# Optimization experiments

Measured on AMD Instinct MI355X. Metric: run time of the kernel, lower is better.

## Reference

```python
import jax, jax.numpy as jnp
import numpy as np

B, N, DIM = 2, 2048, 2048
H, DH = 16, 128            # heads, dim_head; dim_inner = H*DH = 2048
SOFTCAP = 50.0
SCALE = DH ** -0.5


def setup_inputs() -> dict:
    key = jax.random.key(0)
    k1, k2, k3, k4 = jax.random.split(key, 4)
    s = 1.0 / np.sqrt(DIM)
    x = jax.random.normal(k1, (B, N, DIM), dtype=jnp.float32)
    w_qkv = jax.random.normal(k2, (DIM, 3 * H * DH), dtype=jnp.float32) * s
    w_gates = jax.random.normal(k3, (DIM, H), dtype=jnp.float32) * s
    w_out = jax.random.normal(k4, (H * DH, DIM), dtype=jnp.float32) * s
    return {"x": x, "w_qkv": w_qkv, "w_gates": w_gates, "w_out": w_out}


def reference(x, w_qkv, w_gates, w_out):
    b, n, _ = x.shape
    # to_qkv: Linear then 'b n (qkv h d) -> qkv b h n d'
    qkv = (x @ w_qkv).reshape(b, n, 3, H, DH).transpose(2, 0, 3, 1, 4)
    q, k, v = qkv[0], qkv[1], qkv[2]            # each [b, h, n, d]
    q = q * SCALE
    sim = jnp.einsum('bhid,bhjd->bhij', q, k)   # [b, h, n, n]
    sim = jnp.tanh(sim / SOFTCAP) * SOFTCAP     # softclamp
    mask_value = -jnp.finfo(sim.dtype).max
    causal_mask = jnp.triu(jnp.ones((n, n), dtype=bool), 1)
    sim = jnp.where(causal_mask, mask_value, sim)
    attn = jax.nn.softmax(sim, axis=-1)         # dropout = 0.0 (eval)
    out = jnp.einsum('bhij,bhjd->bhid', attn, v)
    # gating: 'b n h -> b h n 1' then sigmoid
    gates = jax.nn.sigmoid(x @ w_gates)         # [b, n, h]
    out = out * gates.transpose(0, 2, 1)[..., None]
    # to_out: 'b h n d -> b n (h d)' then Linear
    out = out.transpose(0, 2, 1, 3).reshape(b, n, H * DH) @ w_out
    return out
```

## Files before the change

### kernel.cpp

```cpp
#include <hip/hip_runtime.h>
#include <hip/hip_bf16.h>
#include <math.h>


typedef __attribute__((ext_vector_type(8))) __bf16 bf16x8;
typedef __attribute__((ext_vector_type(4))) __bf16 bf16x4;
typedef __attribute__((ext_vector_type(4))) float f32x4;

#define MFMA_BF16(a, b, c) __builtin_amdgcn_mfma_f32_16x16x32_bf16((a), (b), (c), 0, 0, 0)

#define NB 2
#define NSEQ 2048
#define NDIM 2048
#define NH 16
#define NDH 128
#define SCALE_Q 0.08838834764831845f

#define AS1 __attribute__((address_space(1)))
#define AS3 __attribute__((address_space(3)))
static __device__ __forceinline__ void gload_lds16(const void* g, void* l) {
  __builtin_amdgcn_global_load_lds((AS1 const void*)g, (AS3 void*)l, 16, 0, 0);
}

static __device__ __forceinline__ unsigned pack2_bf16(float a, float b) {
  unsigned short ua = __builtin_bit_cast(unsigned short, (__bf16)a);
  unsigned short ub = __builtin_bit_cast(unsigned short, (__bf16)b);
  return (unsigned)ua | ((unsigned)ub << 16);
}

__global__ __launch_bounds__(256) void cvt_bf16_kernel(const float* __restrict__ in,
                                                       __bf16* __restrict__ out) {
  int i = blockIdx.x * 256 + threadIdx.x;
  float4 v = reinterpret_cast<const float4*>(in)[i];
  bf16x4 o;
  o[0] = (__bf16)v.x; o[1] = (__bf16)v.y; o[2] = (__bf16)v.z; o[3] = (__bf16)v.w;
  reinterpret_cast<bf16x4*>(out)[i] = o;
}

__global__ __launch_bounds__(256) void transpose_cvt_kernel(const float* __restrict__ in,
                                                            __bf16* __restrict__ out,
                                                            int K, int C) {
  __shared__ float tile[32][33];
  int c0 = blockIdx.x * 32, k0 = blockIdx.y * 32;
  int t = threadIdx.x;
  int lc = t & 31, lr = t >> 5;
#pragma unroll
  for (int rr = 0; rr < 4; ++rr)
    tile[lr + rr * 8][lc] = in[(size_t)(k0 + lr + rr * 8) * C + c0 + lc];
  __syncthreads();
#pragma unroll
  for (int rr = 0; rr < 4; ++rr)
    out[(size_t)(c0 + lr + rr * 8) * K + k0 + lc] = (__bf16)tile[lc][lr + rr * 8];
}

template <int BN> struct SmemG {
  __bf16 A[2][2][128][32];
  __bf16 B[2][2][BN][32];
};

template <int BN>
static __device__ __forceinline__ void stage_half(const __bf16* __restrict__ Ab,
                                                  const __bf16* __restrict__ Bb,
                                                  SmemG<BN>* S, int buf, int ks,
                                                  int kt, int w, int lane) {
  constexpr int LB = BN / 128;
  {
    int gid = w * 64 + lane;
    int row = gid >> 2, gc = gid & 3;
    int sg = gc ^ ((row >> 1) & 3);
    gload_lds16(Ab + (size_t)row * 2048 + kt * 64 + ks * 32 + sg * 8,
                &S->A[buf][ks][0][0] + (size_t)(w * 64) * 8);
  }
#pragma unroll
  for (int j = 0; j < LB; ++j) {
    int gid = j * 512 + w * 64 + lane;
    int row = gid >> 2, gc = gid & 3;
    int sg = gc ^ ((row >> 1) & 3);
    gload_lds16(Bb + (size_t)row * 2048 + kt * 64 + ks * 32 + sg * 8,
                &S->B[buf][ks][0][0] + (size_t)(j * 512 + w * 64) * 8);
  }
}

static __device__ __forceinline__ const bf16x8* fragp(const __bf16* base, int row, int g) {
  return (const bf16x8*)(base + row * 32 + (g ^ ((row >> 1) & 3)) * 8);
}

template <int BN>
static __device__ __forceinline__ void gemm128_core(const __bf16* __restrict__ Abase,
                                                    const __bf16* __restrict__ Bbase,
                                                    SmemG<BN>* S,
                                                    f32x4 (*acc)[BN / 64]) {
  constexpr int NF = BN / 64;
  constexpr int LB = BN / 128;
  int tid = threadIdx.x;
  int w = tid >> 6, lane = tid & 63;
  int ln15 = lane & 15, g = lane >> 4;
  int wr = w >> 2, wc = w & 3;

#pragma unroll
  for (int i = 0; i < 4; ++i)
#pragma unroll
    for (int j = 0; j < NF; ++j) acc[i][j] = (f32x4){0.f, 0.f, 0.f, 0.f};

  stage_half<BN>(Abase, Bbase, S, 0, 0, 0, w, lane);
  stage_half<BN>(Abase, Bbase, S, 0, 1, 0, w, lane);

  for (int t = 0; t < 32; ++t) {
    int bf = t & 1, tb = bf ^ 1;
    int ts = (t < 31) ? t + 1 : 31;
#pragma unroll
    for (int ks = 0; ks < 2; ++ks) {
      stage_half<BN>(Abase, Bbase, S, tb, ks, ts, w, lane);
      if constexpr (LB == 3)
        asm volatile("s_waitcnt vmcnt(8)" ::: "memory");
      else
        asm volatile("s_waitcnt vmcnt(6)" ::: "memory");
      __builtin_amdgcn_s_barrier();
      const __bf16* SA = &S->A[bf][ks][0][0];
      const __bf16* SB = &S->B[bf][ks][0][0];
      bf16x8 af[4], bfr[NF];
#pragma unroll
      for (int nf = 0; nf < NF; ++nf) {
        int row = wc * (BN / 4) + nf * 16 + ln15;
        bfr[nf] = *fragp(SB, row, g);
      }
#pragma unroll
      for (int mf = 0; mf < 4; ++mf) {
        int row = wr * 64 + mf * 16 + ln15;
        af[mf] = *fragp(SA, row, g);
      }
      __builtin_amdgcn_s_setprio(1);
#pragma unroll
      for (int mf = 0; mf < 4; ++mf)
#pragma unroll
        for (int nf = 0; nf < NF; ++nf)
          acc[mf][nf] = MFMA_BF16(af[mf], bfr[nf], acc[mf][nf]);
      __builtin_amdgcn_s_setprio(0);
    }
  }
  asm volatile("s_waitcnt vmcnt(0)" ::: "memory");
}

__global__ __launch_bounds__(512) void gemm_qkv128(const __bf16* __restrict__ A,
                                                   const __bf16* __restrict__ Bt,
                                                   __bf16* __restrict__ qb,
                                                   __bf16* __restrict__ kb,
                                                   __bf16* __restrict__ vtb) {
  __shared__ __align__(1024) SmemG<384> S;
  int sblk = blockIdx.x;
  int x = sblk & 7, i = sblk >> 3;
  int m0 = (i >> 1) * 128;
  int n0 = (2 * x + (i & 1)) * 384;
  f32x4 acc[4][6];
  gemm128_core<384>(A + (size_t)m0 * 2048, Bt + (size_t)n0 * 2048, &S, acc);

  int tid = threadIdx.x;
  int w = tid >> 6, lane = tid & 63;
  int ln15 = lane & 15, g = lane >> 4;
  int wr = w >> 2, wc = w & 3;
#pragma unroll
  for (int nf = 0; nf < 6; ++nf) {
    int ng = n0 + wc * 96 + nf * 16 + ln15;
    int qkv = ng >> 11;
    int h = (ng >> 7) & 15;
    int d = ng & 127;
#pragma unroll
    for (int mf = 0; mf < 4; ++mf)
#pragma unroll
      for (int rr = 0; rr < 4; ++rr) {
        int m = m0 + wr * 64 + mf * 16 + g * 4 + rr;
        int b = m >> 11, n = m & 2047;
        int bh = b * NH + h;
        float v = acc[mf][nf][rr];
        if (qkv == 0)
          qb[((size_t)bh * NSEQ + n) * NDH + d] = (__bf16)(v * SCALE_Q);
        else if (qkv == 1)
          kb[((size_t)bh * NSEQ + n) * NDH + d] = (__bf16)v;
        else
          vtb[((size_t)bh * NDH + d) * NSEQ + n] = (__bf16)v;
      }
  }
}

__global__ __launch_bounds__(512) void gemm_out128(const __bf16* __restrict__ A,
                                                   const __bf16* __restrict__ Bt,
                                                   float* __restrict__ out) {
  __shared__ __align__(1024) SmemG<256> S;
  int sblk = blockIdx.x;
  int x = sblk & 7, i = sblk >> 3;
  int m0 = i * 128;
  int n0 = x * 256;
  f32x4 acc[4][4];
  gemm128_core<256>(A + (size_t)m0 * 2048, Bt + (size_t)n0 * 2048, &S, acc);

  int tid = threadIdx.x;
  int w = tid >> 6, lane = tid & 63;
  int ln15 = lane & 15, g = lane >> 4;
  int wr = w >> 2, wc = w & 3;
#pragma unroll
  for (int mf = 0; mf < 4; ++mf)
#pragma unroll
    for (int nf = 0; nf < 4; ++nf)
#pragma unroll
      for (int rr = 0; rr < 4; ++rr) {
        int m = m0 + wr * 64 + mf * 16 + g * 4 + rr;
        int c = n0 + wc * 64 + nf * 16 + ln15;
        out[(size_t)m * NDIM + c] = acc[mf][nf][rr];
      }
}

__global__ __launch_bounds__(256) void gates_kernel(const float* __restrict__ x,
                                                    const float* __restrict__ wg,
                                                    float* __restrict__ gates) {
  __shared__ float red[64];
  int row = blockIdx.x;
  int tid = threadIdx.x;
  float acc[16];
#pragma unroll
  for (int h = 0; h < 16; ++h) acc[h] = 0.f;
  const float* xr = x + (size_t)row * NDIM;
  for (int k = tid; k < NDIM; k += 256) {
    float xv = xr[k];
    const float* wr = wg + (size_t)k * NH;
#pragma unroll
    for (int h = 0; h < 16; ++h) acc[h] += xv * wr[h];
  }
  int w = tid >> 6, lane = tid & 63;
#pragma unroll
  for (int h = 0; h < 16; ++h) {
    float v = acc[h];
#pragma unroll
    for (int off = 32; off; off >>= 1) v += __shfl_down(v, off);
    if (lane == 0) red[w * 16 + h] = v;
  }
  __syncthreads();
  if (tid < 16) {
    float s = red[tid] + red[16 + tid] + red[32 + tid] + red[48 + tid];
    int b = row >> 11, n = row & 2047;
    gates[((size_t)(b * NH + tid)) * NSEQ + n] = 1.f / (1.f + expf(-s));
  }
}

static __device__ __forceinline__ void softcap_p(const f32x4* accS, float (*p)[4],
                                                 float& l_r, int j0, int q0s,
                                                 bool diag, int ln15, int g) {
#pragma unroll
  for (int jt = 0; jt < 4; ++jt)
#pragma unroll
    for (int r = 0; r < 4; ++r) {
      float e2 = __expf(accS[jt][r] * 0.04f);
      float cap = 50.f - __fdividef(100.f, e2 + 1.f);
      float pv = __expf(cap - 12.f);
      if (diag && (j0 + jt * 16 + g * 4 + r > q0s + ln15)) pv = 0.f;
      p[jt][r] = pv;
      l_r += pv;
    }
}

static __device__ __forceinline__ bf16x8 build_pa(const float (*p)[4], int c,
                                                  int lane_lo, int lane_hi, int g) {
  unsigned P0w0 = pack2_bf16(p[2 * c][0], p[2 * c][1]);
  unsigned P0w1 = pack2_bf16(p[2 * c][2], p[2 * c][3]);
  unsigned P1w0 = pack2_bf16(p[2 * c + 1][0], p[2 * c + 1][1]);
  unsigned P1w1 = pack2_bf16(p[2 * c + 1][2], p[2 * c + 1][3]);
  unsigned a0 = (unsigned)__shfl((int)P0w0, lane_lo);
  unsigned a1 = (unsigned)__shfl((int)P0w1, lane_lo);
  unsigned b0 = (unsigned)__shfl((int)P1w0, lane_lo);
  unsigned b1 = (unsigned)__shfl((int)P1w1, lane_lo);
  unsigned c0 = (unsigned)__shfl((int)P0w0, lane_hi);
  unsigned c1 = (unsigned)__shfl((int)P0w1, lane_hi);
  unsigned e0 = (unsigned)__shfl((int)P1w0, lane_hi);
  unsigned e1 = (unsigned)__shfl((int)P1w1, lane_hi);
  union { unsigned u[4]; bf16x8 v; } pu;
  pu.u[0] = (g < 2) ? a0 : b0;
  pu.u[1] = (g < 2) ? a1 : b1;
  pu.u[2] = (g < 2) ? c0 : e0;
  pu.u[3] = (g < 2) ? c1 : e1;
  return pu.v;
}

static __device__ __forceinline__ void attn_tile2(const __bf16* __restrict__ Kl,
                                                  const __bf16* __restrict__ Vl,
                                                  const bf16x8* qfh, const bf16x8* qfl,
                                                  f32x4* acc_h, f32x4* acc_l,
                                                  float& l_h, float& l_l,
                                                  int j0, int q0h, int q0l,
                                                  bool diag_h, bool diag_l, bool do_lo,
                                                  int ln15, int g) {
  f32x4 sh[4], sl[4];
#pragma unroll
  for (int jt = 0; jt < 4; ++jt) {
    sh[jt] = (f32x4){0.f, 0.f, 0.f, 0.f};
    sl[jt] = (f32x4){0.f, 0.f, 0.f, 0.f};
  }
  __builtin_amdgcn_s_setprio(1);
#pragma unroll
  for (int jt = 0; jt < 4; ++jt)
#pragma unroll
    for (int kc = 0; kc < 4; ++kc) {
      int row = jt * 16 + ln15;
      int bc = (kc * 64 + g * 16) ^ ((row & 7) << 4);
      bf16x8 kf = *reinterpret_cast<const bf16x8*>(Kl + row * 128 + (bc >> 1));
      sh[jt] = MFMA_BF16(kf, qfh[kc], sh[jt]);
      if (do_lo) sl[jt] = MFMA_BF16(kf, qfl[kc], sl[jt]);
    }
  __builtin_amdgcn_s_setprio(0);
  float ph[4][4], pl[4][4];
  softcap_p(sh, ph, l_h, j0, q0h, diag_h, ln15, g);
  if (do_lo) softcap_p(sl, pl, l_l, j0, q0l, diag_l, ln15, g);
  int lane_lo = ln15 + 32 * (g & 1);
  int lane_hi = lane_lo + 16;
#pragma unroll
  for (int c = 0; c < 2; ++c) {
    bf16x8 pah = build_pa(ph, c, lane_lo, lane_hi, g);
    bf16x8 pal = build_pa(pl, c, lane_lo, lane_hi, g);
    __builtin_amdgcn_s_setprio(1);
#pragma unroll
    for (int d0 = 0; d0 < 8; ++d0) {
      int d = d0 * 16 + ln15;
      int bc = (c * 64 + g * 16) ^ ((d & 7) << 4);
      bf16x8 vf = *reinterpret_cast<const bf16x8*>(Vl + d * 64 + (bc >> 1));
      acc_h[d0] = MFMA_BF16(pah, vf, acc_h[d0]);
      if (do_lo) acc_l[d0] = MFMA_BF16(pal, vf, acc_l[d0]);
    }
    __builtin_amdgcn_s_setprio(0);
  }
}

__global__ __launch_bounds__(256, 2) void attn_kernel(const __bf16* __restrict__ qb,
                                                      const __bf16* __restrict__ kb,
                                                      const __bf16* __restrict__ vtb,
                                                      const float* __restrict__ gates,
                                                      __bf16* __restrict__ og) {
  __shared__ __align__(1024) __bf16 Kl[2][64 * 128];
  __shared__ __align__(1024) __bf16 Vl[2][128 * 64];
  int tid = threadIdx.x;
  int w = tid >> 6, lane = tid & 63;
  int ln15 = lane & 15, g = lane >> 4;
  int bx = blockIdx.x;
  int lo = bx & 15, bh = bx >> 4;
  int hi = 31 - lo;
  const __bf16* qh = qb + (size_t)bh * NSEQ * NDH;
  const __bf16* kh = kb + (size_t)bh * NSEQ * NDH;
  const __bf16* vh = vtb + (size_t)bh * NDH * NSEQ;

  int q0h = hi * 64 + w * 16;
  int q0l = lo * 64 + w * 16;
  bf16x8 qfh[4], qfl[4];
#pragma unroll
  for (int kc = 0; kc < 4; ++kc) {
    qfh[kc] = *reinterpret_cast<const bf16x8*>(qh + (size_t)(q0h + ln15) * NDH + kc * 32 + g * 8);
    qfl[kc] = *reinterpret_cast<const bf16x8*>(qh + (size_t)(q0l + ln15) * NDH + kc * 32 + g * 8);
  }

  f32x4 acc_h[8], acc_l[8];
#pragma unroll
  for (int d0 = 0; d0 < 8; ++d0) {
    acc_h[d0] = (f32x4){0.f, 0.f, 0.f, 0.f};
    acc_l[d0] = (f32x4){0.f, 0.f, 0.f, 0.f};
  }
  float l_h = 0.f, l_l = 0.f;

  auto stage = [&](int t, int buf) {
    int j0 = t * 64;
#pragma unroll
    for (int i = 0; i < 4; ++i) {
      int gi = (i * 4 + w) * 64 + lane;
      int kr = gi >> 4, kcs = gi & 15;
      int kc_ = kcs ^ (kr & 7);
      gload_lds16(kh + (size_t)(j0 + kr) * NDH + kc_ * 8, &Kl[buf][(i * 4 + w) * 512]);
      int vr = gi >> 3, vcs = gi & 7;
      int vc_ = vcs ^ (vr & 7);
      gload_lds16(vh + (size_t)vr * NSEQ + j0 + vc_ * 8, &Vl[buf][(i * 4 + w) * 512]);
    }
  };

  stage(0, 0);
  for (int t = 0; t <= hi; ++t) {
    int cb = t & 1;
    if (t < hi) {
      stage(t + 1, cb ^ 1);
      asm volatile("s_waitcnt vmcnt(8)" ::: "memory");
    } else {
      asm volatile("s_waitcnt vmcnt(0)" ::: "memory");
    }
    __builtin_amdgcn_s_barrier();
    attn_tile2(&Kl[cb][0], &Vl[cb][0], qfh, qfl, acc_h, acc_l, l_h, l_l,
               t * 64, q0h, q0l, t == hi, t == lo, t <= lo, ln15, g);
    __builtin_amdgcn_s_barrier();
  }

  l_h += __shfl_xor(l_h, 16); l_h += __shfl_xor(l_h, 32);
  l_l += __shfl_xor(l_l, 16); l_l += __shfl_xor(l_l, 32);

  int b = bh >> 4, h = bh & 15;
#pragma unroll
  for (int set = 0; set < 2; ++set) {
    int q0s = set ? q0l : q0h;
    f32x4* acc = set ? acc_l : acc_h;
    float lr = set ? l_l : l_h;
    float gv[4];
#pragma unroll
    for (int r = 0; r < 4; ++r) {
      float lv = __shfl(lr, g * 4 + r);
      int row = q0s + g * 4 + r;
      gv[r] = gates[(size_t)bh * NSEQ + row] / lv;
    }
#pragma unroll
    for (int d0 = 0; d0 < 8; ++d0)
#pragma unroll
      for (int r = 0; r < 4; ++r) {
        int row = q0s + g * 4 + r;
        og[((size_t)(b * NSEQ + row)) * NDIM + h * NDH + d0 * 16 + ln15] =
            (__bf16)(acc[d0][r] * gv[r]);
      }
  }
}

extern "C" void kernel_launch(void* const* d_in, const int* in_sizes, int n_in,
                              void* d_out, int out_size, void* d_ws, size_t ws_size,
                              hipStream_t stream) {
  const float* x = (const float*)d_in[0];
  const float* w_qkv = (const float*)d_in[1];
  const float* w_gates = (const float*)d_in[2];
  const float* w_out = (const float*)d_in[3];
  float* out = (float*)d_out;
  char* ws = (char*)d_ws;

  __bf16* x_bf   = (__bf16*)(ws + 0);
  __bf16* wqkv_t = (__bf16*)(ws + 16777216);
  __bf16* wout_t = (__bf16*)(ws + 41943040);
  __bf16* q_buf  = (__bf16*)(ws + 50331648);
  __bf16* k_buf  = (__bf16*)(ws + 67108864);
  __bf16* vt_buf = (__bf16*)(ws + 83886080);
  float*  gates  = (float*)(ws + 100663296);
  __bf16* attn_g = (__bf16*)(ws + 100925440);

  cvt_bf16_kernel<<<8192, 256, 0, stream>>>(x, x_bf);
  transpose_cvt_kernel<<<dim3(192, 64), 256, 0, stream>>>(w_qkv, wqkv_t, 2048, 6144);
  transpose_cvt_kernel<<<dim3(64, 64), 256, 0, stream>>>(w_out, wout_t, 2048, 2048);
  gemm_qkv128<<<512, 512, 0, stream>>>(x_bf, wqkv_t, q_buf, k_buf, vt_buf);
  gates_kernel<<<4096, 256, 0, stream>>>(x, w_gates, gates);
  attn_kernel<<<512, 256, 0, stream>>>(q_buf, k_buf, vt_buf, gates, attn_g);
  gemm_out128<<<256, 512, 0, stream>>>(attn_g, wout_t, out);
}
```

Before: 353.7 us.

## Replace QKV GEMM with 256x384 tile and triple-buffered K-32 LDS pipeline

Replaces the 128x384-tile QKV projection GEMM with a new kernel that computes 256x384 tiles (8x6 MFMA fragments per wave) over 256 blocks. It uses a 3-stage ring of 32-wide K slices in LDS, staged with direct global-to-LDS loads two iterations ahead and one barrier per step. The larger M tile halves B-operand reloads per output and the deeper pipeline aims to hide load latency. In exchange it uses more accumulator registers per thread and launches half as many blocks, which may cut occupancy or leave CUs underused.

```diff
diff --git a/kernel.cpp b/kernel.cpp
--- a/kernel.cpp
+++ b/kernel.cpp
@@ -51,6 +51,111 @@
 #pragma unroll
   for (int rr = 0; rr < 4; ++rr)
     out[(size_t)(c0 + lr + rr * 8) * K + k0 + lc] = (__bf16)tile[lc][lr + rr * 8];
+}
+
+struct SmemQ {
+  __bf16 T[3][640][32];
+};
+
+static __device__ __forceinline__ const bf16x8* fragq(const __bf16* base, int row, int g) {
+  return (const bf16x8*)(base + row * 32 + (g ^ ((row >> 1) & 3)) * 8);
+}
+
+__global__ __launch_bounds__(512, 2) void gemm_qkv256b(const __bf16* __restrict__ A,
+                                                       const __bf16* __restrict__ Bt,
+                                                       __bf16* __restrict__ qb,
+                                                       __bf16* __restrict__ kb,
+                                                       __bf16* __restrict__ vtb) {
+  __shared__ __align__(1024) SmemQ S;
+  int sblk = blockIdx.x;
+  int x = sblk & 7, i = sblk >> 3;
+  int m0 = (i >> 1) * 256;
+  int n0 = (2 * x + (i & 1)) * 384;
+  const __bf16* Ab = A + (size_t)m0 * 2048;
+  const __bf16* Bb = Bt + (size_t)n0 * 2048;
+
+  int tid = threadIdx.x;
+  int w = tid >> 6, lane = tid & 63;
+  int ln15 = lane & 15, g = lane >> 4;
+  int wr = w >> 2, wc = w & 3;
+  int lr4 = lane >> 2, l3 = lane & 3;
+
+  auto stage = [&](int kt, int rb) {
+#pragma unroll
+    for (int j = 0; j < 5; ++j) {
+      int k = w + 8 * j;
+      int row = k * 16 + lr4;
+      int sg = l3 ^ ((row >> 1) & 3);
+      const __bf16* src = (k < 16)
+          ? Ab + (size_t)row * 2048 + kt * 32 + sg * 8
+          : Bb + (size_t)(row - 256) * 2048 + kt * 32 + sg * 8;
+      gload_lds16(src, &S.T[rb][k * 16][0]);
+    }
+  };
+
+  f32x4 acc[8][6];
+#pragma unroll
+  for (int a = 0; a < 8; ++a)
+#pragma unroll
+    for (int nf = 0; nf < 6; ++nf) acc[a][nf] = (f32x4){0.f, 0.f, 0.f, 0.f};
+
+  stage(0, 0);
+  stage(1, 1);
+  for (int t = 0; t < 64; ++t) {
+    int rb = t % 3;
+    asm volatile("s_waitcnt vmcnt(5)" ::: "memory");
+    __builtin_amdgcn_s_barrier();
+    asm volatile("" ::: "memory");
+    int ts = (t < 62) ? t + 2 : 63;
+    stage(ts, (t + 2) % 3);
+    const __bf16* Sb = &S.T[rb][0][0];
+    bf16x8 bfr[6];
+#pragma unroll
+    for (int nf = 0; nf < 6; ++nf) {
+      int row = 256 + wc * 96 + nf * 16 + ln15;
+      bfr[nf] = *fragq(Sb, row, g);
+    }
+#pragma unroll
+    for (int mh = 0; mh < 2; ++mh) {
+      bf16x8 af[4];
+#pragma unroll
+      for (int a = 0; a < 4; ++a) {
+        int row = wr * 128 + (mh * 4 + a) * 16 + ln15;
+        af[a] = *fragq(Sb, row, g);
+      }
+      __builtin_amdgcn_s_setprio(1);
+#pragma unroll
+      for (int a = 0; a < 4; ++a)
+#pragma unroll
+        for (int nf = 0; nf < 6; ++nf)
+          acc[mh * 4 + a][nf] = MFMA_BF16(af[a], bfr[nf], acc[mh * 4 + a][nf]);
+      __builtin_amdgcn_s_setprio(0);
+    }
+  }
+  asm volatile("s_waitcnt vmcnt(0)" ::: "memory");
+
+#pragma unroll
+  for (int nf = 0; nf < 6; ++nf) {
+    int ng = n0 + wc * 96 + nf * 16 + ln15;
+    int qkv = ng >> 11;
+    int h = (ng >> 7) & 15;
+    int d = ng & 127;
+#pragma unroll
+    for (int mf = 0; mf < 8; ++mf)
+#pragma unroll
+      for (int rr = 0; rr < 4; ++rr) {
+        int m = m0 + wr * 128 + mf * 16 + g * 4 + rr;
+        int b = m >> 11, n = m & 2047;
+        int bh = b * NH + h;
+        float v = acc[mf][nf][rr];
+        if (qkv == 0)
+          qb[((size_t)bh * NSEQ + n) * NDH + d] = (__bf16)(v * SCALE_Q);
+        else if (qkv == 1)
+          kb[((size_t)bh * NSEQ + n) * NDH + d] = (__bf16)v;
+        else
+          vtb[((size_t)bh * NDH + d) * NSEQ + n] = (__bf16)v;
+      }
+  }
 }
 
 template <int BN> struct SmemG {
@@ -139,47 +244,6 @@
     }
   }
   asm volatile("s_waitcnt vmcnt(0)" ::: "memory");
-}
-
-__global__ __launch_bounds__(512) void gemm_qkv128(const __bf16* __restrict__ A,
-                                                   const __bf16* __restrict__ Bt,
-                                                   __bf16* __restrict__ qb,
-                                                   __bf16* __restrict__ kb,
-                                                   __bf16* __restrict__ vtb) {
-  __shared__ __align__(1024) SmemG<384> S;
-  int sblk = blockIdx.x;
-  int x = sblk & 7, i = sblk >> 3;
-  int m0 = (i >> 1) * 128;
-  int n0 = (2 * x + (i & 1)) * 384;
-  f32x4 acc[4][6];
-  gemm128_core<384>(A + (size_t)m0 * 2048, Bt + (size_t)n0 * 2048, &S, acc);
-
-  int tid = threadIdx.x;
-  int w = tid >> 6, lane = tid & 63;
-  int ln15 = lane & 15, g = lane >> 4;
-  int wr = w >> 2, wc = w & 3;
-#pragma unroll
-  for (int nf = 0; nf < 6; ++nf) {
-    int ng = n0 + wc * 96 + nf * 16 + ln15;
-    int qkv = ng >> 11;
-    int h = (ng >> 7) & 15;
-    int d = ng & 127;
-#pragma unroll
-    for (int mf = 0; mf < 4; ++mf)
-#pragma unroll
-      for (int rr = 0; rr < 4; ++rr) {
-        int m = m0 + wr * 64 + mf * 16 + g * 4 + rr;
-        int b = m >> 11, n = m & 2047;
-        int bh = b * NH + h;
-        float v = acc[mf][nf][rr];
-        if (qkv == 0)
-          qb[((size_t)bh * NSEQ + n) * NDH + d] = (__bf16)(v * SCALE_Q);
-        else if (qkv == 1)
-          kb[((size_t)bh * NSEQ + n) * NDH + d] = (__bf16)v;
-        else
-          vtb[((size_t)bh * NDH + d) * NSEQ + n] = (__bf16)v;
-      }
-  }
 }
 
 __global__ __launch_bounds__(512) void gemm_out128(const __bf16* __restrict__ A,
@@ -439,7 +503,7 @@
   cvt_bf16_kernel<<<8192, 256, 0, stream>>>(x, x_bf);
   transpose_cvt_kernel<<<dim3(192, 64), 256, 0, stream>>>(w_qkv, wqkv_t, 2048, 6144);
   transpose_cvt_kernel<<<dim3(64, 64), 256, 0, stream>>>(w_out, wout_t, 2048, 2048);
-  gemm_qkv128<<<512, 512, 0, stream>>>(x_bf, wqkv_t, q_buf, k_buf, vt_buf);
+  gemm_qkv256b<<<256, 512, 0, stream>>>(x_bf, wqkv_t, q_buf, k_buf, vt_buf);
   gates_kernel<<<4096, 256, 0, stream>>>(x, w_gates, gates);
   attn_kernel<<<512, 256, 0, stream>>>(q_buf, k_buf, vt_buf, gates, attn_g);
   gemm_out128<<<256, 512, 0, stream>>>(attn_g, wout_t, out);
```

Result: faster. 339.8 us (-3.9%).
